# Optimization experiments

Hardware: AMD Instinct MI355X
Metric: run time of the kernel (lower is better)

## Reference

```python
import jax, jax.numpy as jnp
import numpy as np

B, C_IN, H, W = 4, 256, 200, 176
A = 6            # anchors per location (3 sizes x 2 rotations)
NUM_CLS = 4      # 3 classes + background
K = 100
N_ANCH = A * H * W


def setup_inputs() -> dict:
    key = jax.random.key(0)
    k1, k2, k3, k4, k5, k6 = jax.random.split(key, 6)
    x = jax.random.normal(k1, (B, C_IN, H, W), dtype=jnp.float32)
    scale = 1.0 / np.sqrt(C_IN)
    cls_w = jax.random.normal(k2, (NUM_CLS * A, C_IN), dtype=jnp.float32) * scale
    cls_b = jnp.zeros((NUM_CLS * A,), dtype=jnp.float32)
    reg_w = jax.random.normal(k3, (7 * A, C_IN), dtype=jnp.float32) * scale * 0.1
    reg_b = jnp.zeros((7 * A,), dtype=jnp.float32)
    # anchors: [N,7] = (x, y, z, dx, dy, dz, ry) with strictly positive sizes
    xyz = jax.random.uniform(k4, (N_ANCH, 3), minval=-35.0, maxval=35.0)
    sizes = jax.random.uniform(k5, (N_ANCH, 3), minval=1.0, maxval=4.0)
    rot = jax.random.uniform(k6, (N_ANCH, 1), minval=-np.pi, maxval=np.pi)
    anchors = jnp.concatenate([xyz, sizes, rot], axis=-1).astype(jnp.float32)
    return {"x": x, "cls_w": cls_w, "cls_b": cls_b,
            "reg_w": reg_w, "reg_b": reg_b, "anchors": anchors}


def _decode(deltas, anchors):
    # SECOND-style residual box decoder.  deltas, anchors: [B, N, 7]
    xa, ya, za, dxa, dya, dza, ra = jnp.split(anchors, 7, axis=-1)
    xt, yt, zt, dxt, dyt, dzt, rt = jnp.split(deltas, 7, axis=-1)
    diag = jnp.sqrt(dxa * dxa + dya * dya)
    xg = xt * diag + xa
    yg = yt * diag + ya
    zg = zt * dza + za
    dxg = jnp.exp(dxt) * dxa
    dyg = jnp.exp(dyt) * dya
    dzg = jnp.exp(dzt) * dza
    rg = rt + ra
    return jnp.concatenate([xg, yg, zg, dxg, dyg, dzg, rg], axis=-1)


def reference(x, cls_w, cls_b, reg_w, reg_b, anchors):
    # 1x1 conv heads: [B,C_in,H,W] -> [B,C_out,H,W]
    cls_pred = jnp.einsum('bchw,oc->bohw', x, cls_w) + cls_b[None, :, None, None]
    reg_pred = jnp.einsum('bchw,oc->bohw', x, reg_w) + reg_b[None, :, None, None]
    # permute(0,2,3,1).reshape(B, num_anchors, -1)
    cls_pred = jnp.transpose(cls_pred, (0, 2, 3, 1)).reshape(B, N_ANCH, NUM_CLS)
    reg_pred = jnp.transpose(reg_pred, (0, 2, 3, 1)).reshape(B, N_ANCH, 7)
    batch_anchors = jnp.broadcast_to(anchors[None], (B, N_ANCH, 7))
    pred_bboxes = _decode(reg_pred, batch_anchors)
    pred_scores = jax.nn.softmax(cls_pred, axis=-1)
    # per-frame top-k over max foreground score (classes 1:)
    max_scores = jnp.max(pred_scores[..., 1:], axis=-1)      # [B, N]
    _, topk_inds = jax.lax.top_k(max_scores, K)              # [B, K]
    topk_bboxes = jnp.take_along_axis(pred_bboxes, topk_inds[..., None], axis=1)
    topk_scores = jnp.take_along_axis(pred_scores, topk_inds[..., None], axis=1)
    return (topk_scores, topk_bboxes)
```

## Files before the change

### kernel.cpp

```cpp
#include <hip/hip_runtime.h>

#define BB 4
#define CIN 256
#define HW 35200
#define AA 6
#define NANCH (AA * HW)
#define TOPK 100
#define NBIN 4096
#define BINBASE 28416
#define CAP 4096
#define SMAX 4096
#define TILES 138

__device__ __forceinline__ unsigned sbin(unsigned bits) {
  int v = (int)(bits >> 15) - BINBASE;
  v = v < 0 ? 0 : v;
  v = v > (NBIN - 1) ? (NBIN - 1) : v;
  return (unsigned)v;
}

__device__ __forceinline__ float sc4(float4 l) {
  float m = fmaxf(fmaxf(l.x, l.y), fmaxf(l.z, l.w));
  float e0 = expf(l.x - m), e1 = expf(l.y - m);
  float e2 = expf(l.z - m), e3 = expf(l.w - m);
  return fmaxf(fmaxf(e1, e2), e3) / (e0 + e1 + e2 + e3);
}

#define FMA4(A, W, S)                                      \
  A.x = fmaf(S, W.x, A.x); A.y = fmaf(S, W.y, A.y);        \
  A.z = fmaf(S, W.z, A.z); A.w = fmaf(S, W.w, A.w);

__global__ __launch_bounds__(256, 4) void k1_scores(
    const float* __restrict__ x, const float* __restrict__ cls_w,
    const float* __restrict__ cls_b, unsigned int* __restrict__ hist,
    float* __restrict__ maxsc) {
  int bid = blockIdx.x;
  int b = bid / TILES, tile = bid % TILES;
  int tid = threadIdx.x;

  __shared__ __align__(16) float swf[CIN * 24];
  __shared__ unsigned lh[NBIN];
  for (int i = tid; i < CIN * 24; i += 256)
    swf[(i % CIN) * 24 + (i / CIN)] = cls_w[i];
  for (int i = tid; i < NBIN; i += 256) lh[i] = 0;
  __syncthreads();
  const float4* sw4 = (const float4*)swf;

  int hwg = tile * 256 + tid;
  bool act = hwg < HW;
  int hwc = act ? hwg : (HW - 1);
  const float* xb = x + (size_t)b * CIN * HW + hwc;

  float4 a0 = make_float4(cls_b[0], cls_b[1], cls_b[2], cls_b[3]);
  float4 a1 = make_float4(cls_b[4], cls_b[5], cls_b[6], cls_b[7]);
  float4 a2 = make_float4(cls_b[8], cls_b[9], cls_b[10], cls_b[11]);
  float4 a3 = make_float4(cls_b[12], cls_b[13], cls_b[14], cls_b[15]);
  float4 a4 = make_float4(cls_b[16], cls_b[17], cls_b[18], cls_b[19]);
  float4 a5 = make_float4(cls_b[20], cls_b[21], cls_b[22], cls_b[23]);

#pragma unroll 8
  for (int c = 0; c < CIN; ++c) {
    float xv = xb[(size_t)c * HW];
    const float4* wr = sw4 + c * 6;
    float4 w0 = wr[0], w1 = wr[1], w2 = wr[2];
    float4 w3 = wr[3], w4 = wr[4], w5 = wr[5];
    FMA4(a0, w0, xv) FMA4(a1, w1, xv) FMA4(a2, w2, xv)
    FMA4(a3, w3, xv) FMA4(a4, w4, xv) FMA4(a5, w5, xv)
  }

  if (act) {
    float s0 = sc4(a0), s1 = sc4(a1), s2 = sc4(a2);
    float s3 = sc4(a3), s4 = sc4(a4), s5 = sc4(a5);
    float* mp = maxsc + (size_t)b * NANCH + (size_t)hwg * 6u;
    mp[0] = s0; mp[1] = s1; mp[2] = s2; mp[3] = s3; mp[4] = s4; mp[5] = s5;
    atomicAdd(&lh[sbin(__float_as_uint(s0))], 1u);
    atomicAdd(&lh[sbin(__float_as_uint(s1))], 1u);
    atomicAdd(&lh[sbin(__float_as_uint(s2))], 1u);
    atomicAdd(&lh[sbin(__float_as_uint(s3))], 1u);
    atomicAdd(&lh[sbin(__float_as_uint(s4))], 1u);
    atomicAdd(&lh[sbin(__float_as_uint(s5))], 1u);
  }
  __syncthreads();
  unsigned* gh = hist + (size_t)b * NBIN;
  for (int i = tid; i < NBIN; i += 256) {
    unsigned c = lh[i];
    if (c) atomicAdd(&gh[i], c);
  }
}

__global__ __launch_bounds__(256) void k2_thresh(
    const unsigned int* __restrict__ hist, unsigned int* __restrict__ thresh) {
  int b = blockIdx.x, tid = threadIdx.x;
  const unsigned* h = hist + (size_t)b * NBIN;
  unsigned r[16];
  unsigned s = 0;
#pragma unroll
  for (int i = 0; i < 16; ++i) { r[i] = h[tid * 16 + i]; s += r[i]; }
  __shared__ unsigned seg[256];
  seg[tid] = s;
  __syncthreads();
  for (int d = 1; d < 256; d <<= 1) {
    unsigned add = (tid + d < 256) ? seg[tid + d] : 0u;
    __syncthreads();
    seg[tid] += add;
    __syncthreads();
  }
  unsigned above = (tid < 255) ? seg[tid + 1] : 0u;
  if (above < TOPK && above + s >= TOPK) {
    unsigned c = above, T = 0;
    for (int i = 15; i >= 0; --i) {
      c += r[i];
      if (c >= TOPK) { T = tid * 16u + (unsigned)i; break; }
    }
    thresh[b] = T;
  }
}

__global__ __launch_bounds__(256) void k3_compact(
    const float* __restrict__ maxsc, const unsigned int* __restrict__ thresh,
    unsigned int* __restrict__ cand_count, unsigned long long* __restrict__ cand) {
  unsigned p = blockIdx.x * 256u + threadIdx.x;
  unsigned b = p / NANCH, n = p % NANCH;
  unsigned bits = __float_as_uint(maxsc[p]);
  bool pred = sbin(bits) >= thresh[b];
  unsigned long long mask = __ballot(pred);
  if (mask) {
    int lane = threadIdx.x & 63;
    int leader = (int)__ffsll((unsigned long long)mask) - 1;
    unsigned base = 0;
    if (lane == leader)
      base = atomicAdd(&cand_count[b], (unsigned)__popcll(mask));
    base = __shfl(base, leader, 64);
    if (pred) {
      unsigned pos = base + (unsigned)__popcll(mask & ((1ull << lane) - 1ull));
      if (pos < CAP)
        cand[(size_t)b * CAP + pos] =
            ((unsigned long long)bits << 32) | (unsigned)(~n);
    }
  }
}

__global__ __launch_bounds__(256) void k4_sort(
    const unsigned long long* __restrict__ cand,
    const unsigned int* __restrict__ cand_count, unsigned int* __restrict__ topk) {
  int b = blockIdx.x, tid = threadIdx.x;
  __shared__ unsigned long long sh[SMAX];
  unsigned cnt = cand_count[b];
  if (cnt > CAP) cnt = CAP;
  unsigned S = 128;
  while (S < cnt) S <<= 1;
  for (unsigned t = tid; t < S; t += 256)
    sh[t] = (t < cnt) ? cand[(size_t)b * CAP + t] : 0ULL;
  __syncthreads();
  for (unsigned kk = 2; kk <= S; kk <<= 1) {
    for (unsigned jj = kk >> 1; jj > 0; jj >>= 1) {
      for (unsigned t = tid; t < S; t += 256) {
        unsigned ixj = t ^ jj;
        if (ixj > t) {
          unsigned long long a = sh[t], c = sh[ixj];
          bool sw = ((t & kk) == 0) ? (a < c) : (a > c);
          if (sw) { sh[t] = c; sh[ixj] = a; }
        }
      }
      __syncthreads();
    }
  }
  if (tid < TOPK)
    topk[b * TOPK + tid] = ~(unsigned)(sh[tid] & 0xFFFFFFFFULL);
}

__global__ __launch_bounds__(256) void k5_out(
    const float* __restrict__ x, const float* __restrict__ cls_w,
    const float* __restrict__ cls_b, const float* __restrict__ reg_w,
    const float* __restrict__ reg_b, const float* __restrict__ anchors,
    const unsigned int* __restrict__ topk, float* __restrict__ out) {
  int bk = blockIdx.x;
  int b = bk / TOPK, k = bk % TOPK;
  unsigned n = topk[b * TOPK + k];
  int a = (int)(n % AA);
  unsigned hw = n / AA;
  int tid = threadIdx.x;

  float xv = x[(size_t)b * CIN * HW + (size_t)tid * HW + hw];
  float part[11];
#pragma unroll
  for (int j = 0; j < 4; ++j) part[j] = xv * cls_w[(a * 4 + j) * CIN + tid];
#pragma unroll
  for (int j = 0; j < 7; ++j) part[4 + j] = xv * reg_w[(a * 7 + j) * CIN + tid];

#pragma unroll
  for (int j = 0; j < 11; ++j) {
    float v = part[j];
    for (int off = 32; off > 0; off >>= 1) v += __shfl_down(v, off, 64);
    part[j] = v;
  }
  __shared__ float red[4][11];
  int wave = tid >> 6, lane = tid & 63;
  if (lane == 0) {
#pragma unroll
    for (int j = 0; j < 11; ++j) red[wave][j] = part[j];
  }
  __syncthreads();
  if (tid == 0) {
    float tot[11];
#pragma unroll
    for (int j = 0; j < 11; ++j)
      tot[j] = red[0][j] + red[1][j] + red[2][j] + red[3][j];
    float l0 = tot[0] + cls_b[a * 4 + 0];
    float l1 = tot[1] + cls_b[a * 4 + 1];
    float l2 = tot[2] + cls_b[a * 4 + 2];
    float l3 = tot[3] + cls_b[a * 4 + 3];
    float m = fmaxf(fmaxf(l0, l1), fmaxf(l2, l3));
    float e0 = expf(l0 - m), e1 = expf(l1 - m);
    float e2 = expf(l2 - m), e3 = expf(l3 - m);
    float inv = 1.0f / (e0 + e1 + e2 + e3);
    float* os = out + ((size_t)b * TOPK + k) * 4;
    os[0] = e0 * inv; os[1] = e1 * inv; os[2] = e2 * inv; os[3] = e3 * inv;
    const float* an = anchors + (size_t)n * 7;
    float xa = an[0], ya = an[1], za = an[2];
    float dxa = an[3], dya = an[4], dza = an[5], ra = an[6];
    float xt = tot[4] + reg_b[a * 7 + 0];
    float yt = tot[5] + reg_b[a * 7 + 1];
    float zt = tot[6] + reg_b[a * 7 + 2];
    float dxt = tot[7] + reg_b[a * 7 + 3];
    float dyt = tot[8] + reg_b[a * 7 + 4];
    float dzt = tot[9] + reg_b[a * 7 + 5];
    float rt = tot[10] + reg_b[a * 7 + 6];
    float diag = sqrtf(dxa * dxa + dya * dya);
    float* ob = out + (size_t)BB * TOPK * 4 + ((size_t)b * TOPK + k) * 7;
    ob[0] = xt * diag + xa;
    ob[1] = yt * diag + ya;
    ob[2] = zt * dza + za;
    ob[3] = expf(dxt) * dxa;
    ob[4] = expf(dyt) * dya;
    ob[5] = expf(dzt) * dza;
    ob[6] = rt + ra;
  }
}

extern "C" void kernel_launch(void* const* d_in, const int* in_sizes, int n_in,
                              void* d_out, int out_size, void* d_ws, size_t ws_size,
                              hipStream_t stream) {
  const float* x       = (const float*)d_in[0];
  const float* cls_w   = (const float*)d_in[1];
  const float* cls_b   = (const float*)d_in[2];
  const float* reg_w   = (const float*)d_in[3];
  const float* reg_b   = (const float*)d_in[4];
  const float* anchors = (const float*)d_in[5];
  float* out = (float*)d_out;

  char* ws = (char*)d_ws;
  size_t off = 0;
  unsigned int* hist = (unsigned int*)(ws + off);        off += (size_t)BB * NBIN * 4;
  unsigned int* cand_count = (unsigned int*)(ws + off);  off += 64;
  unsigned int* thresh = (unsigned int*)(ws + off);      off += 64;
  unsigned long long* cand = (unsigned long long*)(ws + off); off += (size_t)BB * CAP * 8;
  unsigned int* topk = (unsigned int*)(ws + off);        off += 2048;
  float* maxsc = (float*)(ws + off);

  hipMemsetAsync(hist, 0, (size_t)BB * NBIN * 4 + 64, stream);

  k1_scores<<<BB * TILES, 256, 0, stream>>>(x, cls_w, cls_b, hist, maxsc);
  k2_thresh<<<BB, 256, 0, stream>>>(hist, thresh);
  k3_compact<<<(BB * NANCH) / 256, 256, 0, stream>>>(maxsc, thresh, cand_count, cand);
  k4_sort<<<BB, 256, 0, stream>>>(cand, cand_count, topk);
  k5_out<<<BB * TOPK, 256, 0, stream>>>(x, cls_w, cls_b, reg_w, reg_b, anchors,
                                        topk, out);
}
```

Baseline: 277.9 us.

## Compute four pixels per thread in score kernel with float4 loads

The class-score 1x1 conv kernel now has each thread handle four consecutive spatial positions using float4 loads of x, with 64-thread blocks covering the same 256-pixel tile. Each weight value read from shared memory is reused across four pixels, cutting LDS traffic per FMA. The cost is 96 accumulator registers, only one wavefront per block, and fewer waves to hide memory latency. The active check requires all four pixels to be in range, which holds because HW is a multiple of 4.

New measurement: 282.7 us. Within noise of the previous version (+1.7%).

```diff
diff --git a/kernel.cpp b/kernel.cpp
--- a/kernel.cpp
+++ b/kernel.cpp
@@ -26,11 +26,27 @@
   return fmaxf(fmaxf(e1, e2), e3) / (e0 + e1 + e2 + e3);
 }
 
-#define FMA4(A, W, S)                                      \
-  A.x = fmaf(S, W.x, A.x); A.y = fmaf(S, W.y, A.y);        \
-  A.z = fmaf(S, W.z, A.z); A.w = fmaf(S, W.w, A.w);
-
-__global__ __launch_bounds__(256, 4) void k1_scores(
+#define DQ(i) float4 q##i = make_float4(cls_b[i], cls_b[i], cls_b[i], cls_b[i]);
+#define FM(Q, WS)                                          \
+  Q.x = fmaf(xv.x, WS, Q.x); Q.y = fmaf(xv.y, WS, Q.y);    \
+  Q.z = fmaf(xv.z, WS, Q.z); Q.w = fmaf(xv.w, WS, Q.w);
+#define SC(F, Qa, Qb, Qc, Qd) sc4(make_float4(Qa F, Qb F, Qc F, Qd F))
+#define DOPOS(F, PP)                                                       \
+  {                                                                        \
+    float t0 = SC(F, q0, q1, q2, q3), t1 = SC(F, q4, q5, q6, q7);          \
+    float t2 = SC(F, q8, q9, q10, q11), t3 = SC(F, q12, q13, q14, q15);    \
+    float t4 = SC(F, q16, q17, q18, q19), t5 = SC(F, q20, q21, q22, q23);  \
+    mp[PP * 6 + 0] = t0; mp[PP * 6 + 1] = t1; mp[PP * 6 + 2] = t2;         \
+    mp[PP * 6 + 3] = t3; mp[PP * 6 + 4] = t4; mp[PP * 6 + 5] = t5;         \
+    atomicAdd(&lh[sbin(__float_as_uint(t0))], 1u);                         \
+    atomicAdd(&lh[sbin(__float_as_uint(t1))], 1u);                         \
+    atomicAdd(&lh[sbin(__float_as_uint(t2))], 1u);                         \
+    atomicAdd(&lh[sbin(__float_as_uint(t3))], 1u);                         \
+    atomicAdd(&lh[sbin(__float_as_uint(t4))], 1u);                         \
+    atomicAdd(&lh[sbin(__float_as_uint(t5))], 1u);                         \
+  }
+
+__global__ __launch_bounds__(64, 2) void k1_scores(
     const float* __restrict__ x, const float* __restrict__ cls_w,
     const float* __restrict__ cls_b, unsigned int* __restrict__ hist,
     float* __restrict__ maxsc) {
@@ -40,49 +56,42 @@
 
   __shared__ __align__(16) float swf[CIN * 24];
   __shared__ unsigned lh[NBIN];
-  for (int i = tid; i < CIN * 24; i += 256)
-    swf[(i % CIN) * 24 + (i / CIN)] = cls_w[i];
-  for (int i = tid; i < NBIN; i += 256) lh[i] = 0;
+  for (int i = tid; i < CIN * 24; i += 64)
+    swf[(i & 255) * 24 + (i >> 8)] = cls_w[i];
+  for (int i = tid; i < NBIN; i += 64) lh[i] = 0;
   __syncthreads();
   const float4* sw4 = (const float4*)swf;
 
-  int hwg = tile * 256 + tid;
-  bool act = hwg < HW;
-  int hwc = act ? hwg : (HW - 1);
+  int hw0 = tile * 256 + tid * 4;
+  bool act = hw0 <= HW - 4;
+  int hwc = act ? hw0 : 0;
   const float* xb = x + (size_t)b * CIN * HW + hwc;
 
-  float4 a0 = make_float4(cls_b[0], cls_b[1], cls_b[2], cls_b[3]);
-  float4 a1 = make_float4(cls_b[4], cls_b[5], cls_b[6], cls_b[7]);
-  float4 a2 = make_float4(cls_b[8], cls_b[9], cls_b[10], cls_b[11]);
-  float4 a3 = make_float4(cls_b[12], cls_b[13], cls_b[14], cls_b[15]);
-  float4 a4 = make_float4(cls_b[16], cls_b[17], cls_b[18], cls_b[19]);
-  float4 a5 = make_float4(cls_b[20], cls_b[21], cls_b[22], cls_b[23]);
-
-#pragma unroll 8
+  DQ(0) DQ(1) DQ(2) DQ(3) DQ(4) DQ(5) DQ(6) DQ(7)
+  DQ(8) DQ(9) DQ(10) DQ(11) DQ(12) DQ(13) DQ(14) DQ(15)
+  DQ(16) DQ(17) DQ(18) DQ(19) DQ(20) DQ(21) DQ(22) DQ(23)
+
+#pragma unroll 4
   for (int c = 0; c < CIN; ++c) {
-    float xv = xb[(size_t)c * HW];
+    float4 xv = *(const float4*)(xb + (size_t)c * HW);
     const float4* wr = sw4 + c * 6;
     float4 w0 = wr[0], w1 = wr[1], w2 = wr[2];
     float4 w3 = wr[3], w4 = wr[4], w5 = wr[5];
-    FMA4(a0, w0, xv) FMA4(a1, w1, xv) FMA4(a2, w2, xv)
-    FMA4(a3, w3, xv) FMA4(a4, w4, xv) FMA4(a5, w5, xv)
+    FM(q0, w0.x) FM(q1, w0.y) FM(q2, w0.z) FM(q3, w0.w)
+    FM(q4, w1.x) FM(q5, w1.y) FM(q6, w1.z) FM(q7, w1.w)
+    FM(q8, w2.x) FM(q9, w2.y) FM(q10, w2.z) FM(q11, w2.w)
+    FM(q12, w3.x) FM(q13, w3.y) FM(q14, w3.z) FM(q15, w3.w)
+    FM(q16, w4.x) FM(q17, w4.y) FM(q18, w4.z) FM(q19, w4.w)
+    FM(q20, w5.x) FM(q21, w5.y) FM(q22, w5.z) FM(q23, w5.w)
   }
 
   if (act) {
-    float s0 = sc4(a0), s1 = sc4(a1), s2 = sc4(a2);
-    float s3 = sc4(a3), s4 = sc4(a4), s5 = sc4(a5);
-    float* mp = maxsc + (size_t)b * NANCH + (size_t)hwg * 6u;
-    mp[0] = s0; mp[1] = s1; mp[2] = s2; mp[3] = s3; mp[4] = s4; mp[5] = s5;
-    atomicAdd(&lh[sbin(__float_as_uint(s0))], 1u);
-    atomicAdd(&lh[sbin(__float_as_uint(s1))], 1u);
-    atomicAdd(&lh[sbin(__float_as_uint(s2))], 1u);
-    atomicAdd(&lh[sbin(__float_as_uint(s3))], 1u);
-    atomicAdd(&lh[sbin(__float_as_uint(s4))], 1u);
-    atomicAdd(&lh[sbin(__float_as_uint(s5))], 1u);
+    float* mp = maxsc + (size_t)b * NANCH + (size_t)hw0 * 6u;
+    DOPOS(.x, 0) DOPOS(.y, 1) DOPOS(.z, 2) DOPOS(.w, 3)
   }
   __syncthreads();
   unsigned* gh = hist + (size_t)b * NBIN;
-  for (int i = tid; i < NBIN; i += 256) {
+  for (int i = tid; i < NBIN; i += 64) {
     unsigned c = lh[i];
     if (c) atomicAdd(&gh[i], c);
   }
@@ -260,7 +269,7 @@
 
   hipMemsetAsync(hist, 0, (size_t)BB * NBIN * 4 + 64, stream);
 
-  k1_scores<<<BB * TILES, 256, 0, stream>>>(x, cls_w, cls_b, hist, maxsc);
+  k1_scores<<<BB * TILES, 64, 0, stream>>>(x, cls_w, cls_b, hist, maxsc);
   k2_thresh<<<BB, 256, 0, stream>>>(hist, thresh);
   k3_compact<<<(BB * NANCH) / 256, 256, 0, stream>>>(maxsc, thresh, cand_count, cand);
   k4_sort<<<BB, 256, 0, stream>>>(cand, cand_count, topk);
```

## Split channel reduction across waves and coarsen score histogram bins

Applied to the files above, without the earlier changes.

The cls 1x1-conv kernel now has each wave handle a quarter of the input channels for four pixels per lane, accumulating 96 partial sums in registers. The partials are then reduced through a new shared-memory buffer before softmax and histogramming. This raises per-thread ILP and cuts the per-channel shared weight loads per pixel, at the cost of more registers (launch bounds lowered to 2 blocks), extra LDS, and four serialized sync stages. The histogram is also halved to 2048 coarser bins, which shrinks histogram work but may let more candidates pass the threshold into compaction.

Result: slower. 299.0 us (+7.6%).

```diff
diff --git a/kernel.cpp b/kernel.cpp
--- a/kernel.cpp
+++ b/kernel.cpp
@@ -6,79 +6,96 @@
 #define AA 6
 #define NANCH (AA * HW)
 #define TOPK 100
-#define NBIN 4096
-#define BINBASE 28416
+#define NBIN 2048
+#define BINBASE 14208
 #define CAP 4096
 #define SMAX 4096
 #define TILES 138
 
 __device__ __forceinline__ unsigned sbin(unsigned bits) {
-  int v = (int)(bits >> 15) - BINBASE;
+  int v = (int)(bits >> 16) - BINBASE;
   v = v < 0 ? 0 : v;
   v = v > (NBIN - 1) ? (NBIN - 1) : v;
   return (unsigned)v;
 }
 
-__device__ __forceinline__ float sc4(float4 l) {
-  float m = fmaxf(fmaxf(l.x, l.y), fmaxf(l.z, l.w));
-  float e0 = expf(l.x - m), e1 = expf(l.y - m);
-  float e2 = expf(l.z - m), e3 = expf(l.w - m);
-  return fmaxf(fmaxf(e1, e2), e3) / (e0 + e1 + e2 + e3);
-}
-
-#define FMA4(A, W, S)                                      \
-  A.x = fmaf(S, W.x, A.x); A.y = fmaf(S, W.y, A.y);        \
-  A.z = fmaf(S, W.z, A.z); A.w = fmaf(S, W.w, A.w);
-
-__global__ __launch_bounds__(256, 4) void k1_scores(
+#define DA(o) float4 A##o = make_float4(0.f, 0.f, 0.f, 0.f);
+#define FMP(o, WS)                                          \
+  A##o.x = fmaf(xv0, WS, A##o.x); A##o.y = fmaf(xv1, WS, A##o.y); \
+  A##o.z = fmaf(xv2, WS, A##o.z); A##o.w = fmaf(xv3, WS, A##o.w);
+#define REDS(o) { int ib = o * 256 + lane; red[ib] = A##o.x;        \
+  red[ib + 64] = A##o.y; red[ib + 128] = A##o.z; red[ib + 192] = A##o.w; }
+#define REDA(o) { int ib = o * 256 + lane; red[ib] += A##o.x;       \
+  red[ib + 64] += A##o.y; red[ib + 128] += A##o.z; red[ib + 192] += A##o.w; }
+#define RED_ALL(M) M(0) M(1) M(2) M(3) M(4) M(5) M(6) M(7) M(8) M(9) M(10) \
+  M(11) M(12) M(13) M(14) M(15) M(16) M(17) M(18) M(19) M(20) M(21) M(22) M(23)
+
+__global__ __launch_bounds__(256, 2) void k1_scores(
     const float* __restrict__ x, const float* __restrict__ cls_w,
     const float* __restrict__ cls_b, unsigned int* __restrict__ hist,
     float* __restrict__ maxsc) {
   int bid = blockIdx.x;
   int b = bid / TILES, tile = bid % TILES;
-  int tid = threadIdx.x;
+  int tid = threadIdx.x, wave = tid >> 6, lane = tid & 63;
 
   __shared__ __align__(16) float swf[CIN * 24];
+  __shared__ float red[24 * 256];
   __shared__ unsigned lh[NBIN];
   for (int i = tid; i < CIN * 24; i += 256)
-    swf[(i % CIN) * 24 + (i / CIN)] = cls_w[i];
+    swf[(i & 255) * 24 + (i >> 8)] = cls_w[i];
   for (int i = tid; i < NBIN; i += 256) lh[i] = 0;
   __syncthreads();
   const float4* sw4 = (const float4*)swf;
 
-  int hwg = tile * 256 + tid;
-  bool act = hwg < HW;
-  int hwc = act ? hwg : (HW - 1);
-  const float* xb = x + (size_t)b * CIN * HW + hwc;
-
-  float4 a0 = make_float4(cls_b[0], cls_b[1], cls_b[2], cls_b[3]);
-  float4 a1 = make_float4(cls_b[4], cls_b[5], cls_b[6], cls_b[7]);
-  float4 a2 = make_float4(cls_b[8], cls_b[9], cls_b[10], cls_b[11]);
-  float4 a3 = make_float4(cls_b[12], cls_b[13], cls_b[14], cls_b[15]);
-  float4 a4 = make_float4(cls_b[16], cls_b[17], cls_b[18], cls_b[19]);
-  float4 a5 = make_float4(cls_b[20], cls_b[21], cls_b[22], cls_b[23]);
-
-#pragma unroll 8
-  for (int c = 0; c < CIN; ++c) {
-    float xv = xb[(size_t)c * HW];
-    const float4* wr = sw4 + c * 6;
+  int pbase = tile * 256 + lane;
+  int o0 = pbase            < HW ? pbase       : HW - 1;
+  int o1 = pbase + 64       < HW ? pbase + 64  : HW - 1;
+  int o2 = pbase + 128      < HW ? pbase + 128 : HW - 1;
+  int o3 = pbase + 192      < HW ? pbase + 192 : HW - 1;
+  const float* xw = x + (size_t)b * CIN * HW + (size_t)(wave * 64) * HW;
+
+  RED_ALL(DA)
+
+#pragma unroll 4
+  for (int c = 0; c < 64; ++c) {
+    const float* xc = xw + (size_t)c * HW;
+    float xv0 = xc[o0], xv1 = xc[o1], xv2 = xc[o2], xv3 = xc[o3];
+    const float4* wr = sw4 + (wave * 64 + c) * 6;
     float4 w0 = wr[0], w1 = wr[1], w2 = wr[2];
     float4 w3 = wr[3], w4 = wr[4], w5 = wr[5];
-    FMA4(a0, w0, xv) FMA4(a1, w1, xv) FMA4(a2, w2, xv)
-    FMA4(a3, w3, xv) FMA4(a4, w4, xv) FMA4(a5, w5, xv)
-  }
-
-  if (act) {
-    float s0 = sc4(a0), s1 = sc4(a1), s2 = sc4(a2);
-    float s3 = sc4(a3), s4 = sc4(a4), s5 = sc4(a5);
+    FMP(0, w0.x) FMP(1, w0.y) FMP(2, w0.z) FMP(3, w0.w)
+    FMP(4, w1.x) FMP(5, w1.y) FMP(6, w1.z) FMP(7, w1.w)
+    FMP(8, w2.x) FMP(9, w2.y) FMP(10, w2.z) FMP(11, w2.w)
+    FMP(12, w3.x) FMP(13, w3.y) FMP(14, w3.z) FMP(15, w3.w)
+    FMP(16, w4.x) FMP(17, w4.y) FMP(18, w4.z) FMP(19, w4.w)
+    FMP(20, w5.x) FMP(21, w5.y) FMP(22, w5.z) FMP(23, w5.w)
+  }
+
+  if (wave == 0) { RED_ALL(REDS) }
+  __syncthreads();
+  if (wave == 1) { RED_ALL(REDA) }
+  __syncthreads();
+  if (wave == 2) { RED_ALL(REDA) }
+  __syncthreads();
+  if (wave == 3) { RED_ALL(REDA) }
+  __syncthreads();
+
+  int hwg = tile * 256 + tid;
+  if (hwg < HW) {
     float* mp = maxsc + (size_t)b * NANCH + (size_t)hwg * 6u;
-    mp[0] = s0; mp[1] = s1; mp[2] = s2; mp[3] = s3; mp[4] = s4; mp[5] = s5;
-    atomicAdd(&lh[sbin(__float_as_uint(s0))], 1u);
-    atomicAdd(&lh[sbin(__float_as_uint(s1))], 1u);
-    atomicAdd(&lh[sbin(__float_as_uint(s2))], 1u);
-    atomicAdd(&lh[sbin(__float_as_uint(s3))], 1u);
-    atomicAdd(&lh[sbin(__float_as_uint(s4))], 1u);
-    atomicAdd(&lh[sbin(__float_as_uint(s5))], 1u);
+#pragma unroll
+    for (int a = 0; a < AA; ++a) {
+      float l0 = red[(a * 4 + 0) * 256 + tid] + cls_b[a * 4 + 0];
+      float l1 = red[(a * 4 + 1) * 256 + tid] + cls_b[a * 4 + 1];
+      float l2 = red[(a * 4 + 2) * 256 + tid] + cls_b[a * 4 + 2];
+      float l3 = red[(a * 4 + 3) * 256 + tid] + cls_b[a * 4 + 3];
+      float m = fmaxf(fmaxf(l0, l1), fmaxf(l2, l3));
+      float e0 = expf(l0 - m), e1 = expf(l1 - m);
+      float e2 = expf(l2 - m), e3 = expf(l3 - m);
+      float s = fmaxf(fmaxf(e1, e2), e3) / (e0 + e1 + e2 + e3);
+      mp[a] = s;
+      atomicAdd(&lh[sbin(__float_as_uint(s))], 1u);
+    }
   }
   __syncthreads();
   unsigned* gh = hist + (size_t)b * NBIN;
@@ -92,10 +109,10 @@
     const unsigned int* __restrict__ hist, unsigned int* __restrict__ thresh) {
   int b = blockIdx.x, tid = threadIdx.x;
   const unsigned* h = hist + (size_t)b * NBIN;
-  unsigned r[16];
+  unsigned r[8];
   unsigned s = 0;
 #pragma unroll
-  for (int i = 0; i < 16; ++i) { r[i] = h[tid * 16 + i]; s += r[i]; }
+  for (int i = 0; i < 8; ++i) { r[i] = h[tid * 8 + i]; s += r[i]; }
   __shared__ unsigned seg[256];
   seg[tid] = s;
   __syncthreads();
@@ -108,9 +125,9 @@
   unsigned above = (tid < 255) ? seg[tid + 1] : 0u;
   if (above < TOPK && above + s >= TOPK) {
     unsigned c = above, T = 0;
-    for (int i = 15; i >= 0; --i) {
+    for (int i = 7; i >= 0; --i) {
       c += r[i];
-      if (c >= TOPK) { T = tid * 16u + (unsigned)i; break; }
+      if (c >= TOPK) { T = tid * 8u + (unsigned)i; break; }
     }
     thresh[b] = T;
   }
```
